# Kernel optimization log

Measured on AMD Instinct MI355X. Metric: run time of the kernel, lower is better.

Reference implementation:

```python
import jax, jax.numpy as jnp
import numpy as np

jax.config.update("jax_enable_x64", True)

SR = 24000
NCH = 64
F_MIN, F_MAX = 10.0, 100.0
R_MIN, R_MAX = 0.9999, 0.99999
ALIGN_W, RAW_W = 10.0, 0.1
FFT_CFG = [(512, 128), (1024, 256), (2048, 512)]  # (n_fft==win_length, hop)
EPS = 1e-7

# deterministic IIR coefficients (buffers in the torch module)
_freqs = np.exp(np.linspace(np.log(F_MIN), np.log(F_MAX), NCH))
_radii = np.linspace(R_MIN, R_MAX, NCH)
_theta = 2.0 * np.pi * _freqs / SR
A1 = jnp.asarray(-2.0 * _radii * np.cos(_theta), jnp.float64)  # [C]
A2 = jnp.asarray(_radii ** 2, jnp.float64)                      # [C]
B0 = jnp.asarray((1.0 - _radii) * 0.5, jnp.float64)             # [C]


def _iir(x):
    # x: [B,1,T] float32 -> causal 2nd-order IIR per channel in float64 -> [B,C,T] float32
    B, _, T = x.shape
    xd = jnp.broadcast_to(x.astype(jnp.float64), (B, NCH, T))
    xt = jnp.moveaxis(xd, 2, 0)  # [T,B,C]
    z = jnp.zeros((B, NCH), jnp.float64)

    def step(carry, xn):
        y1, y2 = carry
        y = B0 * xn - A1 * y1 - A2 * y2  # y[n] = b0*x[n] - a1*y[n-1] - a2*y[n-2]
        return (y, y1), y

    _, ys = jax.lax.scan(step, (z, z), xt)
    return jnp.moveaxis(ys, 0, 2).astype(jnp.float32)  # [B,C,T]


def _probe(x):
    fwd = _iir(x)
    bwd = jnp.flip(_iir(jnp.flip(x, axis=-1)), axis=-1)
    return jnp.concatenate([fwd, bwd], axis=1)  # [B,2C,T]


def _stft_mag(x1d, n_fft, hop):
    # torch.stft(center=False, window=None) == rectangular frames + rfft
    T = x1d.shape[-1]
    n_frames = 1 + (T - n_fft) // hop
    idx = np.arange(n_frames)[:, None] * hop + np.arange(n_fft)[None, :]
    frames = x1d[:, idx]  # [B, n_frames, n_fft]
    return jnp.abs(jnp.fft.rfft(frames, axis=-1)) + EPS


def _mss_loss(pred, target):
    loss = jnp.float32(0.0)
    xp, xt = pred[:, 0, :], target[:, 0, :]
    for n_fft, hop in FFT_CFG:
        xm = _stft_mag(xp, n_fft, hop)
        ym = _stft_mag(xt, n_fft, hop)
        loss = loss + jnp.mean(jnp.abs(xm - ym)) + jnp.mean(jnp.abs(jnp.log(xm) - jnp.log(ym)))
    return loss


def setup_inputs() -> dict:
    key = jax.random.key(0)
    k1, k2, k3 = jax.random.split(key, 3)
    pred = jax.random.normal(k1, (4, 1, 48000), dtype=jnp.float32)
    target = jax.random.normal(k2, (4, 1, 48000), dtype=jnp.float32)
    # orthogonal init of the frozen Tank mixing matrix [out=64, in=128]
    g = jax.random.normal(k3, (128, 64), dtype=jnp.float32)
    q, _ = jnp.linalg.qr(g)
    W = q.T.astype(jnp.float32)  # [64,128], rows orthonormal
    return {"pred": pred, "target": target, "W": W}


def reference(pred, target, W):
    T = pred.shape[-1]
    m = T // 3
    l_mss = _mss_loss(pred, target)

    tank = lambda h: jnp.tanh(jnp.einsum('bct,oc->bot', h, W))  # Linear on [B,T,2C] then tanh
    p_emb = tank(_probe(pred))
    t_emb = tank(_probe(target))
    l_align = jnp.mean(jnp.abs(p_emb[..., m:-m] - t_emb[..., m:-m]))
    l_raw = jnp.mean(jnp.abs(pred[..., m:-m] - target[..., m:-m])) * RAW_W
    total = l_mss + l_align * ALIGN_W + l_raw
    return (total, l_mss, l_align)
```

## Files before the change

kernel.cpp:

```cpp
#include <hip/hip_runtime.h>

#define T_LEN 48000
#define NSEQ  1024
#define LC    100
#define NCHK  320
#define GRP   16
#define NGRP  20

#define NB_F2048 360
#define NB_F1024 736
#define NB_F512  1488
#define NB_FFT   2584
#define NB_P1    1280
#define NB_EMB   250

using short8 = __attribute__((ext_vector_type(8))) short;
using f32x4  = __attribute__((ext_vector_type(4))) float;

__device__ __forceinline__ void chan_params(int ch, double& a1, double& a2, double& b0) {
    const double lf = log(10.0) + (double)ch * (log(100.0) - log(10.0)) / 63.0;
    const double f  = exp(lf);
    const double r  = 0.9999 + (double)ch * (0.99999 - 0.9999) / 63.0;
    const double th = 2.0 * 3.14159265358979323846 * f / 24000.0;
    a1 = -2.0 * r * cos(th);
    a2 = r * r;
    b0 = (1.0 - r) * 0.5;
}

__device__ __forceinline__ unsigned short f32_to_bf16(float f) {
    unsigned u = __float_as_uint(f);
    u += 0x7fffu + ((u >> 16) & 1u);
    return (unsigned short)(u >> 16);
}

__device__ __forceinline__ float fast_tanh(float x) {
    const float e = __expf(2.0f * x);
    return 1.0f - 2.0f / (e + 1.0f);
}

__device__ __forceinline__ float2 cmul(float2 a, float2 b) {
    return make_float2(a.x * b.x - a.y * b.y, a.x * b.y + a.y * b.x);
}
__device__ __forceinline__ float2 cadd(float2 a, float2 b) { return make_float2(a.x + b.x, a.y + b.y); }
__device__ __forceinline__ float2 csub(float2 a, float2 b) { return make_float2(a.x - b.x, a.y - b.y); }

__global__ void setup_kernel(double* __restrict__ cst) {
    const int t = threadIdx.x;
    if (t < 64) {
        double a1, a2, b0; chan_params(t, a1, a2, b0);
        double m00 = -a1, m01 = -a2, m10 = 1.0, m11 = 0.0;
        double r00 = 1.0, r01 = 0.0, r10 = 0.0, r11 = 1.0;
        int e = LC;
        while (e) {
            if (e & 1) {
                const double t00 = r00 * m00 + r01 * m10, t01 = r00 * m01 + r01 * m11;
                const double t10 = r10 * m00 + r11 * m10, t11 = r10 * m01 + r11 * m11;
                r00 = t00; r01 = t01; r10 = t10; r11 = t11;
            }
            const double q00 = m00 * m00 + m01 * m10, q01 = m00 * m01 + m01 * m11;
            const double q10 = m10 * m00 + m11 * m10, q11 = m10 * m01 + m11 * m11;
            m00 = q00; m01 = q01; m10 = q10; m11 = q11;
            e >>= 1;
        }
        cst[t * 16 + 0] = a1; cst[t * 16 + 1] = a2; cst[t * 16 + 2] = b0;
        cst[t * 16 + 3] = r00; cst[t * 16 + 4] = r01;
        cst[t * 16 + 5] = r10; cst[t * 16 + 6] = r11;
        double q00 = r00, q01 = r01, q10 = r10, q11 = r11;
        #pragma unroll
        for (int s = 0; s < 4; ++s) {
            const double n00 = q00 * q00 + q01 * q10, n01 = q00 * q01 + q01 * q11;
            const double n10 = q10 * q00 + q11 * q10, n11 = q10 * q01 + q11 * q11;
            q00 = n00; q01 = n01; q10 = n10; q11 = n11;
        }
        cst[t * 16 + 7] = q00; cst[t * 16 + 8]  = q01;
        cst[t * 16 + 9] = q10; cst[t * 16 + 10] = q11;
    }
}

__global__ __launch_bounds__(256) void phase1_kernel(const float* __restrict__ pred,
                                                     const float* __restrict__ target,
                                                     const double* __restrict__ cst,
                                                     float2* __restrict__ P,
                                                     double* __restrict__ fftP) {
    __shared__ float2 bufA[2048];
    __shared__ float2 bufB[2048];
    __shared__ float2 twl[512];
    __shared__ float redw[8];
    const int blk = blockIdx.x;

    if (blk < NB_FFT) {
        int N, HOP, id;
        double scale;
        if (blk < NB_F2048)                  { N = 2048; HOP = 512; id = blk;
                                               scale = 1.0 / (4.0 * 90.0 * 1025.0); }
        else if (blk < NB_F2048 + NB_F1024)  { N = 1024; HOP = 256; id = blk - NB_F2048;
                                               scale = 1.0 / (4.0 * 184.0 * 513.0); }
        else                                 { N = 512;  HOP = 128; id = blk - NB_F2048 - NB_F1024;
                                               scale = 1.0 / (4.0 * 372.0 * 257.0); }
        const int tid = threadIdx.x;
        const int b   = id & 3;
        const int fr  = id >> 2;
        const int N4  = N >> 2;
        const float* xp = pred   + b * T_LEN + fr * HOP;
        const float* xt = target + b * T_LEN + fr * HOP;

        const float wstep = -6.283185307179586f / (float)N;
        for (int k = tid; k < N4; k += 256) {
            float sn, cs; __sincosf(wstep * (float)k, &sn, &cs);
            twl[k] = make_float2(cs, sn);
        }
        for (int i = tid; i < N; i += 256) bufA[i] = make_float2(xp[i], xt[i]);
        __syncthreads();

        float2* X = bufA; float2* Y = bufB;
        int s = 1, ls = 0;
        while ((s << 2) <= N) {
            for (int i = tid; i < N4; i += 256) {
                const int p  = i >> ls;
                const int q  = i & (s - 1);
                const int k1 = p << ls;
                const float2 a0 = X[i];
                const float2 a1 = X[i + N4];
                const float2 a2 = X[i + 2 * N4];
                const float2 a3 = X[i + 3 * N4];
                const float2 w1 = twl[k1];
                const int   k2 = k1 << 1;
                const float2 t2 = twl[k2 & (N4 - 1)];
                const float2 w2 = (k2 < N4) ? t2 : make_float2(t2.y, -t2.x);
                const float2 e1 = cadd(a0, a2), d1 = csub(a0, a2);
                const float2 e2 = cadd(a1, a3), d2 = csub(a1, a3);
                const float2 o1 = cmul(d1, w1);
                const float2 ot = cmul(d2, w1);
                const float2 o2 = make_float2(ot.y, -ot.x);
                const float2 E1 = cadd(e1, e2);
                const float2 O1 = cmul(csub(e1, e2), w2);
                const float2 E2 = cadd(o1, o2);
                const float2 O2 = cmul(csub(o1, o2), w2);
                const int o4 = q + (p << (ls + 2));
                Y[o4]         = E1;
                Y[o4 + s]     = E2;
                Y[o4 + 2 * s] = O1;
                Y[o4 + 3 * s] = O2;
            }
            __syncthreads();
            float2* t = X; X = Y; Y = t;
            s <<= 2; ls += 2;
        }
        const bool rad2 = (s < N);
        const int  half = N >> 1;

        float s1 = 0.f, s2 = 0.f;
        for (int k = tid; k <= half; k += 256) {
            const int k2 = (N - k) & (N - 1);
            float2 zk, zn;
            if (rad2) {
                zk = (k  < half) ? cadd(X[k],  X[k  + half]) : csub(X[k  - half], X[k]);
                zn = (k2 < half) ? cadd(X[k2], X[k2 + half]) : csub(X[k2 - half], X[k2]);
            } else {
                zk = X[k]; zn = X[k2];
            }
            const float xpr = 0.5f * (zk.x + zn.x), xpi = 0.5f * (zk.y - zn.y);
            const float xtr = 0.5f * (zk.y + zn.y), xti = 0.5f * (zn.x - zk.x);
            const float xm = sqrtf(xpr * xpr + xpi * xpi) + 1e-7f;
            const float ym = sqrtf(xtr * xtr + xti * xti) + 1e-7f;
            s1 += fabsf(xm - ym);
            s2 += fabsf(__logf(xm) - __logf(ym));
        }
        for (int off = 32; off >= 1; off >>= 1) {
            s1 += __shfl_down(s1, off, 64);
            s2 += __shfl_down(s2, off, 64);
        }
        const int lane = tid & 63, wv = tid >> 6;
        if (lane == 0) { redw[wv] = s1; redw[wv + 4] = s2; }
        __syncthreads();
        if (tid == 0) {
            const double t1 = (double)redw[0] + (double)redw[1] + (double)redw[2] + (double)redw[3];
            const double t2 = (double)redw[4] + (double)redw[5] + (double)redw[6] + (double)redw[7];
            fftP[blk] = (t1 + t2) * scale;
        }
        return;
    }

    const int tid   = (blk - NB_FFT) * 256 + threadIdx.x;
    const int seq   = tid & (NSEQ - 1);
    const int chunk = tid >> 10;
    const int ch  = seq & 63;
    const int dir = (seq >> 6) & 1;
    const int b   = (seq >> 7) & 3;
    const int sg  = seq >> 9;
    const double a1 = cst[ch * 16 + 0], a2 = cst[ch * 16 + 1], b0 = cst[ch * 16 + 2];
    const float* x = (sg ? target : pred) + b * T_LEN;
    const int n0   = chunk * LC;
    const int base = dir ? (T_LEN - 1 - n0) : n0;
    const int stp  = dir ? -1 : 1;
    double y1 = 0.0, y2 = 0.0;
    #pragma unroll 4
    for (int i = 0; i < LC; ++i) {
        const double xv = (double)x[base + stp * i];
        const double y  = b0 * xv - a1 * y1 - a2 * y2;
        y2 = y1; y1 = y;
    }
    P[chunk * NSEQ + seq] = make_float2((float)y1, (float)y2);
}

__global__ __launch_bounds__(256) void iir_scanA(const double* __restrict__ cst,
                                                 const float2* __restrict__ P,
                                                 float2* __restrict__ Tg) {
    const int tid = blockIdx.x * 256 + threadIdx.x;
    const int seq = tid & (NSEQ - 1);
    const int g   = tid >> 10;
    const int ch  = seq & 63;
    const double A00 = cst[ch * 16 + 3], A01 = cst[ch * 16 + 4];
    const double A10 = cst[ch * 16 + 5], A11 = cst[ch * 16 + 6];
    double t1 = 0.0, t2 = 0.0;
    #pragma unroll
    for (int j = 0; j < GRP; ++j) {
        const float2 p = P[(g * GRP + j) * NSEQ + seq];
        const double n1 = A00 * t1 + A01 * t2 + (double)p.x;
        const double n2 = A10 * t1 + A11 * t2 + (double)p.y;
        t1 = n1; t2 = n2;
    }
    Tg[g * NSEQ + seq] = make_float2((float)t1, (float)t2);
}

__global__ __launch_bounds__(256) void iir_pass2(const float* __restrict__ pred,
                                                 const float* __restrict__ target,
                                                 const double* __restrict__ cst,
                                                 const float2* __restrict__ P,
                                                 const float2* __restrict__ Tg,
                                                 unsigned short* __restrict__ H) {
    const int tid = blockIdx.x * 256 + threadIdx.x;
    const int seq = tid & (NSEQ - 1);
    const int c   = 160 + (tid >> 10);
    const int ch  = seq & 63;
    const int dir = (seq >> 6) & 1;
    const int b   = (seq >> 7) & 3;
    const int sg  = seq >> 9;
    const double a1 = cst[ch * 16 + 0], a2 = cst[ch * 16 + 1], b0 = cst[ch * 16 + 2];
    const double A00 = cst[ch * 16 + 3], A01 = cst[ch * 16 + 4];
    const double A10 = cst[ch * 16 + 5], A11 = cst[ch * 16 + 6];
    const double B00 = cst[ch * 16 + 7], B01 = cst[ch * 16 + 8];
    const double B10 = cst[ch * 16 + 9], B11 = cst[ch * 16 + 10];

    const int g = c >> 4;
    double y1 = 0.0, y2 = 0.0;
    for (int j = 0; j < g; ++j) {
        const float2 t = Tg[j * NSEQ + seq];
        const double n1 = B00 * y1 + B01 * y2 + (double)t.x;
        const double n2 = B10 * y1 + B11 * y2 + (double)t.y;
        y1 = n1; y2 = n2;
    }
    for (int k = g * GRP; k < c; ++k) {
        const float2 p = P[k * NSEQ + seq];
        const double n1 = A00 * y1 + A01 * y2 + (double)p.x;
        const double n2 = A10 * y1 + A11 * y2 + (double)p.y;
        y1 = n1; y2 = n2;
    }

    const float* x = (sg ? target : pred) + b * T_LEN;
    const int n0 = c * LC;
    unsigned short* Hb = H + (size_t)(sg * 4 + b) * 16000 * 128 + (dir * 64 + ch);
    if (dir == 0) {
        #pragma unroll 4
        for (int i = 0; i < LC; ++i) {
            const int n = n0 + i;
            const double xv = (double)x[n];
            const double y  = b0 * xv - a1 * y1 - a2 * y2;
            Hb[(size_t)(n - 16000) * 128] = f32_to_bf16((float)y);
            y2 = y1; y1 = y;
        }
    } else {
        #pragma unroll 4
        for (int i = 0; i < LC; ++i) {
            const int n = n0 + i;
            const double xv = (double)x[T_LEN - 1 - n];
            const double y  = b0 * xv - a1 * y1 - a2 * y2;
            Hb[(size_t)(31999 - n) * 128] = f32_to_bf16((float)y);
            y2 = y1; y1 = y;
        }
    }
}

__global__ __launch_bounds__(256) void embed_kernel(const float* __restrict__ W,
                                                    const unsigned short* __restrict__ H,
                                                    const float* __restrict__ pred,
                                                    const float* __restrict__ target,
                                                    double2* __restrict__ emP) {
    __shared__ double em[8];
    float rsum;
    {
        const int i  = blockIdx.x * 256 + threadIdx.x;
        const int bb = i / 16000;
        const int t  = i - bb * 16000 + 16000;
        rsum = fabsf(pred[bb * T_LEN + t] - target[bb * T_LEN + t]);
        for (int off = 32; off >= 1; off >>= 1) rsum += __shfl_down(rsum, off, 64);
    }

    const int lane = threadIdx.x & 63;
    const int wave = threadIdx.x >> 6;
    const int gw   = blockIdx.x * 4 + wave;
    const int row  = lane & 15;
    const int quad = lane >> 4;

    short8 A[4][4];
    #pragma unroll
    for (int mi = 0; mi < 4; ++mi)
        #pragma unroll
        for (int ki = 0; ki < 4; ++ki) {
            const float* wp = W + (mi * 16 + row) * 128 + ki * 32 + quad * 8;
            short8 a;
            #pragma unroll
            for (int j = 0; j < 8; ++j) a[j] = (short)f32_to_bf16(wp[j]);
            A[mi][ki] = a;
        }

    float lsum = 0.f;
    const int t0 = gw * 16;
    for (int b = 0; b < 4; ++b) {
        const unsigned short* hp = H + (size_t)(b * 16000 + t0 + row) * 128 + quad * 8;
        const unsigned short* ht = hp + (size_t)4 * 16000 * 128;
        f32x4 accp[4], acct[4];
        #pragma unroll
        for (int mi = 0; mi < 4; ++mi) {
            accp[mi] = f32x4{0.f, 0.f, 0.f, 0.f};
            acct[mi] = f32x4{0.f, 0.f, 0.f, 0.f};
        }
        #pragma unroll
        for (int ki = 0; ki < 4; ++ki) {
            const short8 bp = *(const short8*)(hp + ki * 32);
            const short8 bt = *(const short8*)(ht + ki * 32);
            #pragma unroll
            for (int mi = 0; mi < 4; ++mi) {
                accp[mi] = __builtin_amdgcn_mfma_f32_16x16x32_bf16(A[mi][ki], bp, accp[mi], 0, 0, 0);
                acct[mi] = __builtin_amdgcn_mfma_f32_16x16x32_bf16(A[mi][ki], bt, acct[mi], 0, 0, 0);
            }
        }
        #pragma unroll
        for (int mi = 0; mi < 4; ++mi)
            #pragma unroll
            for (int r = 0; r < 4; ++r) {
                const float ep = fast_tanh(accp[mi][r]);
                const float et = fast_tanh(acct[mi][r]);
                lsum += fabsf(ep - et);
            }
    }
    for (int off = 32; off >= 1; off >>= 1) lsum += __shfl_down(lsum, off, 64);
    if (lane == 0) { em[wave] = (double)lsum; em[wave + 4] = (double)rsum; }
    __syncthreads();
    if (threadIdx.x == 0)
        emP[blockIdx.x] = make_double2(em[0] + em[1] + em[2] + em[3],
                                       em[4] + em[5] + em[6] + em[7]);
}

__global__ __launch_bounds__(256) void finalize_kernel(const double* __restrict__ fftP,
                                                       const double2* __restrict__ emP,
                                                       float* __restrict__ out) {
    __shared__ double red[256];
    const int tid = threadIdx.x;
    double lm = 0.0;
    for (int i = tid; i < NB_FFT; i += 256) lm += fftP[i];
    double la = 0.0, lr = 0.0;
    for (int i = tid; i < NB_EMB; i += 256) { const double2 e = emP[i]; la += e.x; lr += e.y; }

    red[tid] = lm; __syncthreads();
    for (int o = 128; o > 0; o >>= 1) { if (tid < o) red[tid] += red[tid + o]; __syncthreads(); }
    lm = red[0]; __syncthreads();
    red[tid] = la; __syncthreads();
    for (int o = 128; o > 0; o >>= 1) { if (tid < o) red[tid] += red[tid + o]; __syncthreads(); }
    la = red[0]; __syncthreads();
    red[tid] = lr; __syncthreads();
    for (int o = 128; o > 0; o >>= 1) { if (tid < o) red[tid] += red[tid + o]; __syncthreads(); }
    if (tid == 0) {
        lr = red[0] / 64000.0 * 0.1;
        la = la / (4.0 * 64.0 * 16000.0);
        out[0] = (float)(lm + 10.0 * la + lr);
        out[1] = (float)lm;
        out[2] = (float)la;
    }
}

extern "C" void kernel_launch(void* const* d_in, const int* in_sizes, int n_in,
                              void* d_out, int out_size, void* d_ws, size_t ws_size,
                              hipStream_t stream) {
    const float* pred   = (const float*)d_in[0];
    const float* target = (const float*)d_in[1];
    const float* W      = (const float*)d_in[2];
    float* out = (float*)d_out;

    char* ws = (char*)d_ws;
    double*  cst  = (double*)ws;
    double*  fftP = (double*)(ws + 8192);
    double2* emP  = (double2*)(ws + 28928);
    float2*  P    = (float2*)(ws + 33280);
    float2*  Tg   = (float2*)(ws + 2654720);
    unsigned short* H = (unsigned short*)(ws + 2818560);

    hipLaunchKernelGGL(setup_kernel,  dim3(1), dim3(64), 0, stream, cst);
    hipLaunchKernelGGL(phase1_kernel, dim3(NB_FFT + NB_P1), dim3(256), 0, stream, pred, target, cst, P, fftP);
    hipLaunchKernelGGL(iir_scanA,     dim3(NGRP * 4), dim3(256), 0, stream, cst, P, Tg);
    hipLaunchKernelGGL(iir_pass2,     dim3(640), dim3(256), 0, stream, pred, target, cst, P, Tg, H);
    hipLaunchKernelGGL(embed_kernel,  dim3(NB_EMB), dim3(256), 0, stream, W, H, pred, target, emP);
    hipLaunchKernelGGL(finalize_kernel, dim3(1), dim3(256), 0, stream, fftP, emP, out);
}
```

Before: 133.8 us.

## Pack two 512-point FFT frames per block and run IIR chunks in fp32

The 512-point STFT frames are now processed two per block, 128 threads each, using separate halves of shared memory. This halves the number of small FFT blocks and the launch work they carry. The per-chunk IIR recurrences in phase1 and the final chunk scan now run in float instead of double, which reduces FP64 cost, while the chunk-carry matrix propagation stays in double. The risk is accuracy: poles very near unit radius in fp32 over 100-sample chunks may drift from the float64 reference. The merged reduction of the two loss terms also changes summation order slightly.

```diff
diff --git a/kernel.cpp b/kernel.cpp
--- a/kernel.cpp
+++ b/kernel.cpp
@@ -9,10 +9,11 @@
 
 #define NB_F2048 360
 #define NB_F1024 736
-#define NB_F512  1488
-#define NB_FFT   2584
+#define NB_F512  744
+#define NB_FFT   1840
 #define NB_P1    1280
 #define NB_EMB   250
+#define NFRAMES  2584
 
 using short8 = __attribute__((ext_vector_type(8))) short;
 using f32x4  = __attribute__((ext_vector_type(4))) float;
@@ -85,22 +86,32 @@
     __shared__ float2 bufA[2048];
     __shared__ float2 bufB[2048];
     __shared__ float2 twl[512];
-    __shared__ float redw[8];
+    __shared__ float redw[4];
     const int blk = blockIdx.x;
 
     if (blk < NB_FFT) {
-        int N, HOP, id;
+        int N, HOP, frame0, nthr, lt, off;
         double scale;
-        if (blk < NB_F2048)                  { N = 2048; HOP = 512; id = blk;
-                                               scale = 1.0 / (4.0 * 90.0 * 1025.0); }
-        else if (blk < NB_F2048 + NB_F1024)  { N = 1024; HOP = 256; id = blk - NB_F2048;
-                                               scale = 1.0 / (4.0 * 184.0 * 513.0); }
-        else                                 { N = 512;  HOP = 128; id = blk - NB_F2048 - NB_F1024;
-                                               scale = 1.0 / (4.0 * 372.0 * 257.0); }
         const int tid = threadIdx.x;
-        const int b   = id & 3;
-        const int fr  = id >> 2;
-        const int N4  = N >> 2;
+        if (blk < NB_F2048) {
+            N = 2048; HOP = 512; scale = 1.0 / (4.0 * 90.0 * 1025.0);
+            frame0 = blk; nthr = 256; lt = tid; off = 0;
+        } else if (blk < NB_F2048 + NB_F1024) {
+            N = 1024; HOP = 256; scale = 1.0 / (4.0 * 184.0 * 513.0);
+            frame0 = blk; nthr = 256; lt = tid; off = 0;
+        } else {
+            N = 512;  HOP = 128; scale = 1.0 / (4.0 * 372.0 * 257.0);
+            const int id = blk - (NB_F2048 + NB_F1024);
+            frame0 = NB_F2048 + NB_F1024 + 2 * id + (tid >> 7);
+            nthr = 128; lt = tid & 127; off = (tid >> 7) << 9;
+        }
+        int fidL;
+        if (blk < NB_F2048) fidL = frame0;
+        else if (blk < NB_F2048 + NB_F1024) fidL = frame0 - NB_F2048;
+        else fidL = frame0 - (NB_F2048 + NB_F1024);
+        const int b  = fidL & 3;
+        const int fr = fidL >> 2;
+        const int N4 = N >> 2;
         const float* xp = pred   + b * T_LEN + fr * HOP;
         const float* xt = target + b * T_LEN + fr * HOP;
 
@@ -109,20 +120,20 @@
             float sn, cs; __sincosf(wstep * (float)k, &sn, &cs);
             twl[k] = make_float2(cs, sn);
         }
-        for (int i = tid; i < N; i += 256) bufA[i] = make_float2(xp[i], xt[i]);
+        for (int i = lt; i < N; i += nthr) bufA[off + i] = make_float2(xp[i], xt[i]);
         __syncthreads();
 
         float2* X = bufA; float2* Y = bufB;
         int s = 1, ls = 0;
         while ((s << 2) <= N) {
-            for (int i = tid; i < N4; i += 256) {
+            for (int i = lt; i < N4; i += nthr) {
                 const int p  = i >> ls;
                 const int q  = i & (s - 1);
                 const int k1 = p << ls;
-                const float2 a0 = X[i];
-                const float2 a1 = X[i + N4];
-                const float2 a2 = X[i + 2 * N4];
-                const float2 a3 = X[i + 3 * N4];
+                const float2 a0 = X[off + i];
+                const float2 a1 = X[off + i + N4];
+                const float2 a2 = X[off + i + 2 * N4];
+                const float2 a3 = X[off + i + 3 * N4];
                 const float2 w1 = twl[k1];
                 const int   k2 = k1 << 1;
                 const float2 t2 = twl[k2 & (N4 - 1)];
@@ -137,10 +148,10 @@
                 const float2 E2 = cadd(o1, o2);
                 const float2 O2 = cmul(csub(o1, o2), w2);
                 const int o4 = q + (p << (ls + 2));
-                Y[o4]         = E1;
-                Y[o4 + s]     = E2;
-                Y[o4 + 2 * s] = O1;
-                Y[o4 + 3 * s] = O2;
+                Y[off + o4]         = E1;
+                Y[off + o4 + s]     = E2;
+                Y[off + o4 + 2 * s] = O1;
+                Y[off + o4 + 3 * s] = O2;
             }
             __syncthreads();
             float2* t = X; X = Y; Y = t;
@@ -149,34 +160,34 @@
         const bool rad2 = (s < N);
         const int  half = N >> 1;
 
-        float s1 = 0.f, s2 = 0.f;
-        for (int k = tid; k <= half; k += 256) {
+        float ss = 0.f;
+        for (int k = lt; k <= half; k += nthr) {
             const int k2 = (N - k) & (N - 1);
             float2 zk, zn;
             if (rad2) {
-                zk = (k  < half) ? cadd(X[k],  X[k  + half]) : csub(X[k  - half], X[k]);
-                zn = (k2 < half) ? cadd(X[k2], X[k2 + half]) : csub(X[k2 - half], X[k2]);
+                zk = (k  < half) ? cadd(X[off + k],  X[off + k  + half]) : csub(X[off + k  - half], X[off + k]);
+                zn = (k2 < half) ? cadd(X[off + k2], X[off + k2 + half]) : csub(X[off + k2 - half], X[off + k2]);
             } else {
-                zk = X[k]; zn = X[k2];
+                zk = X[off + k]; zn = X[off + k2];
             }
             const float xpr = 0.5f * (zk.x + zn.x), xpi = 0.5f * (zk.y - zn.y);
             const float xtr = 0.5f * (zk.y + zn.y), xti = 0.5f * (zn.x - zk.x);
             const float xm = sqrtf(xpr * xpr + xpi * xpi) + 1e-7f;
             const float ym = sqrtf(xtr * xtr + xti * xti) + 1e-7f;
-            s1 += fabsf(xm - ym);
-            s2 += fabsf(__logf(xm) - __logf(ym));
-        }
-        for (int off = 32; off >= 1; off >>= 1) {
-            s1 += __shfl_down(s1, off, 64);
-            s2 += __shfl_down(s2, off, 64);
-        }
+            ss += fabsf(xm - ym) + fabsf(__logf(xm) - __logf(ym));
+        }
+        for (int o = 32; o >= 1; o >>= 1) ss += __shfl_down(ss, o, 64);
         const int lane = tid & 63, wv = tid >> 6;
-        if (lane == 0) { redw[wv] = s1; redw[wv + 4] = s2; }
+        if (lane == 0) redw[wv] = ss;
         __syncthreads();
-        if (tid == 0) {
-            const double t1 = (double)redw[0] + (double)redw[1] + (double)redw[2] + (double)redw[3];
-            const double t2 = (double)redw[4] + (double)redw[5] + (double)redw[6] + (double)redw[7];
-            fftP[blk] = (t1 + t2) * scale;
+        if (nthr == 256) {
+            if (tid == 0)
+                fftP[frame0] = ((double)redw[0] + (double)redw[1] +
+                                (double)redw[2] + (double)redw[3]) * scale;
+        } else {
+            if (lt == 0)
+                fftP[frame0] = ((double)redw[(tid >> 7) * 2] +
+                                (double)redw[(tid >> 7) * 2 + 1]) * scale;
         }
         return;
     }
@@ -188,19 +199,21 @@
     const int dir = (seq >> 6) & 1;
     const int b   = (seq >> 7) & 3;
     const int sg  = seq >> 9;
-    const double a1 = cst[ch * 16 + 0], a2 = cst[ch * 16 + 1], b0 = cst[ch * 16 + 2];
+    const float a1f = (float)cst[ch * 16 + 0];
+    const float a2f = (float)cst[ch * 16 + 1];
+    const float b0f = (float)cst[ch * 16 + 2];
     const float* x = (sg ? target : pred) + b * T_LEN;
     const int n0   = chunk * LC;
     const int base = dir ? (T_LEN - 1 - n0) : n0;
     const int stp  = dir ? -1 : 1;
-    double y1 = 0.0, y2 = 0.0;
+    float y1 = 0.f, y2 = 0.f;
     #pragma unroll 4
     for (int i = 0; i < LC; ++i) {
-        const double xv = (double)x[base + stp * i];
-        const double y  = b0 * xv - a1 * y1 - a2 * y2;
+        const float xv = x[base + stp * i];
+        const float y  = b0f * xv - a1f * y1 - a2f * y2;
         y2 = y1; y1 = y;
     }
-    P[chunk * NSEQ + seq] = make_float2((float)y1, (float)y2);
+    P[chunk * NSEQ + seq] = make_float2(y1, y2);
 }
 
 __global__ __launch_bounds__(256) void iir_scanA(const double* __restrict__ cst,
@@ -236,7 +249,6 @@
     const int dir = (seq >> 6) & 1;
     const int b   = (seq >> 7) & 3;
     const int sg  = seq >> 9;
-    const double a1 = cst[ch * 16 + 0], a2 = cst[ch * 16 + 1], b0 = cst[ch * 16 + 2];
     const double A00 = cst[ch * 16 + 3], A01 = cst[ch * 16 + 4];
     const double A10 = cst[ch * 16 + 5], A11 = cst[ch * 16 + 6];
     const double B00 = cst[ch * 16 + 7], B01 = cst[ch * 16 + 8];
@@ -257,6 +269,10 @@
         y1 = n1; y2 = n2;
     }
 
+    const float a1f = (float)cst[ch * 16 + 0];
+    const float a2f = (float)cst[ch * 16 + 1];
+    const float b0f = (float)cst[ch * 16 + 2];
+    float y1f = (float)y1, y2f = (float)y2;
     const float* x = (sg ? target : pred) + b * T_LEN;
     const int n0 = c * LC;
     unsigned short* Hb = H + (size_t)(sg * 4 + b) * 16000 * 128 + (dir * 64 + ch);
@@ -264,19 +280,19 @@
         #pragma unroll 4
         for (int i = 0; i < LC; ++i) {
             const int n = n0 + i;
-            const double xv = (double)x[n];
-            const double y  = b0 * xv - a1 * y1 - a2 * y2;
-            Hb[(size_t)(n - 16000) * 128] = f32_to_bf16((float)y);
-            y2 = y1; y1 = y;
+            const float xv = x[n];
+            const float y  = b0f * xv - a1f * y1f - a2f * y2f;
+            Hb[(size_t)(n - 16000) * 128] = f32_to_bf16(y);
+            y2f = y1f; y1f = y;
         }
     } else {
         #pragma unroll 4
         for (int i = 0; i < LC; ++i) {
             const int n = n0 + i;
-            const double xv = (double)x[T_LEN - 1 - n];
-            const double y  = b0 * xv - a1 * y1 - a2 * y2;
-            Hb[(size_t)(31999 - n) * 128] = f32_to_bf16((float)y);
-            y2 = y1; y1 = y;
+            const float xv = x[T_LEN - 1 - n];
+            const float y  = b0f * xv - a1f * y1f - a2f * y2f;
+            Hb[(size_t)(31999 - n) * 128] = f32_to_bf16(y);
+            y2f = y1f; y1f = y;
         }
     }
 }
@@ -358,7 +374,7 @@
     __shared__ double red[256];
     const int tid = threadIdx.x;
     double lm = 0.0;
-    for (int i = tid; i < NB_FFT; i += 256) lm += fftP[i];
+    for (int i = tid; i < NFRAMES; i += 256) lm += fftP[i];
     double la = 0.0, lr = 0.0;
     for (int i = tid; i < NB_EMB; i += 256) { const double2 e = emP[i]; la += e.x; lr += e.y; }
 
```

Result: faster. 126.4 us (-5.5%).
